# Optimization experiments

Hardware: AMD Instinct MI355X
Metric: run time of the kernel (lower is better)

Reference implementation:

```python
import jax, jax.numpy as jnp
import numpy as np

N_QUBITS = 14
N_LAYERS = 6
BATCH = 512
DIM = 2 ** N_QUBITS

# Z expectation sign table: qubit 0 is the most-significant bit of the state index
_idx = np.arange(DIM)
_bits = np.stack([(_idx >> (N_QUBITS - 1 - q)) & 1 for q in range(N_QUBITS)])  # [n, DIM]
SIGNS = jnp.asarray(1.0 - 2.0 * _bits, dtype=jnp.float32)  # +1 for bit 0, -1 for bit 1


def _rx(theta):
    # 2x2 RX(theta) = [[cos(t/2), -i sin(t/2)], [-i sin(t/2), cos(t/2)]]
    c = jnp.cos(theta / 2).astype(jnp.complex64)
    s = ((-1j) * jnp.sin(theta / 2)).astype(jnp.complex64)
    return jnp.stack([jnp.stack([c, s]), jnp.stack([s, c])])


def _apply_1q(state, mat, q):
    # state: [B, 2^n] complex; apply 2x2 mat on qubit q
    left = 2 ** q
    right = 2 ** (N_QUBITS - 1 - q)
    s = state.reshape(-1, left, 2, right)
    s = jnp.einsum('ij,bljr->blir', mat, s)
    return s.reshape(-1, DIM)


def _apply_cnot(state, c, t):
    # CNOT(control=c, target=t): flip target bit where control bit is 1
    hi, lo = (c, t) if c < t else (t, c)
    A = 2 ** hi
    M = 2 ** (lo - hi - 1)
    R = 2 ** (N_QUBITS - 1 - lo)
    s = state.reshape(-1, A, 2, M, 2, R)
    if c < t:
        flipped = jnp.flip(s[:, :, 1:2, :, :, :], axis=4)
        s = jnp.concatenate([s[:, :, 0:1, :, :, :], flipped], axis=2)
    else:
        flipped = jnp.flip(s[:, :, :, :, 1:2, :], axis=2)
        s = jnp.concatenate([s[:, :, :, :, 0:1, :], flipped], axis=4)
    return s.reshape(-1, DIM)


def _forward(x, params):
    B = x.shape[0]
    # angle embedding in X basis: product state of RX(x_q)|0> per qubit
    half = 0.5 * x
    amps = jnp.stack([jnp.cos(half).astype(jnp.complex64),
                      ((-1j) * jnp.sin(half)).astype(jnp.complex64)], axis=-1)  # [B, n, 2]
    state = amps[:, 0]
    for q in range(1, N_QUBITS):
        state = (state[:, :, None] * amps[:, q][:, None, :]).reshape(B, -1)
    # basic_entangling ansatz: per-qubit RX then ring of CNOTs, per layer
    for layer in range(N_LAYERS):
        w = params[layer, 0]  # [n_qubits]
        for q in range(N_QUBITS):
            state = _apply_1q(state, _rx(w[q]), q)
        for q in range(N_QUBITS):
            state = _apply_cnot(state, q, (q + 1) % N_QUBITS)
    # <Z_q> expectation per qubit
    probs = state.real ** 2 + state.imag ** 2  # [B, DIM]
    return probs @ SIGNS.T  # [B, n_qubits]


def setup_inputs():
    key = jax.random.key(0)
    k1, k2 = jax.random.split(key)
    x = jax.random.normal(k1, (BATCH, N_QUBITS), dtype=jnp.float32)
    params = 2.0 * jnp.pi * jax.random.uniform(k2, (N_LAYERS, 1, N_QUBITS), dtype=jnp.float32)
    return {"x": x, "params": params}


def reference(x, params):
    return _forward(x, params)
```

## Files before the change

kernel.cpp:

```cpp
#include <hip/hip_runtime.h>
#include <math.h>


#define NQ 14
#define DIM 16384
#define NLAYERS 6
#define NGATES (NLAYERS * NQ)
#define BATCH 512
#define TB 1024
#define NREP 16
#define NSLICE 16
#define SLICE_B (BATCH / NSLICE)
#define B_PER_WAVE (SLICE_B * 64 / TB)
static_assert(B_PER_WAVE == 2, "phase B hand-unrolled for 2 batches/wave");

constexpr int cpopc(unsigned v) { int c = 0; while (v) { c += (int)(v & 1u); v >>= 1; } return c; }

constexpr unsigned cpext(unsigned v, unsigned m) {
    unsigned r = 0; int b = 0;
    for (int pos = 0; pos < 16; ++pos)
        if ((m >> pos) & 1u) { r |= ((v >> pos) & 1u) << b; ++b; }
    return r;
}

struct Tabs {
    unsigned short m[NGATES];
    unsigned short r[NQ];
    int p[NQ];
    int off[NQ + 1];
    unsigned char qb[NQ][NQ];
    int ng[NQ];
    unsigned short gmask[NQ][NGATES];
    unsigned char  gidx[NQ][NGATES];
};

constexpr Tabs gen_tabs() {
    Tabs T{};
    unsigned short C[NQ] = {}, R[NQ] = {};
    for (int q = 0; q < NQ; ++q) { C[q] = (unsigned short)(1u << (NQ - 1 - q)); R[q] = C[q]; }
    for (int l = 0; l < NLAYERS; ++l) {
        for (int q = 0; q < NQ; ++q) T.m[l * NQ + q] = C[q];
        for (int g = 0; g < NQ; ++g) {
            int t = (g + 1) % NQ;
            C[g] ^= C[t];
            R[t] ^= R[g];
        }
    }
    for (int q = 0; q < NQ; ++q) T.r[q] = R[q];
    for (int q = 0; q < NQ; ++q) {
        int cnt = 0;
        for (int pos = 0; pos < NQ; ++pos)
            if ((R[q] >> pos) & 1u) { T.qb[q][cnt] = (unsigned char)(NQ - 1 - pos); ++cnt; }
        T.p[q] = cnt;
    }
    T.off[0] = 0;
    for (int q = 0; q < NQ; ++q) T.off[q + 1] = T.off[q] + (1 << T.p[q]);
    for (int q = 0; q < NQ; ++q) {
        int n = 0;
        for (int g = 0; g < NGATES; ++g) {
            if (cpopc((unsigned)(T.m[g] & R[q])) & 1) {
                T.gmask[q][n] = T.m[g];
                T.gidx[q][n]  = (unsigned char)g;
                ++n;
            }
        }
        T.ng[q] = n;
    }
    return T;
}
constexpr Tabs TAB = gen_tabs();

constexpr int calc_maxp() { int m = 0; for (int q = 0; q < NQ; ++q) if (TAB.p[q] > m) m = TAB.p[q]; return m; }
constexpr int calc_minp() { int m = 99; for (int q = 0; q < NQ; ++q) if (TAB.p[q] < m) m = TAB.p[q]; return m; }
constexpr int MAXP  = calc_maxp();
constexpr int MINP  = calc_minp();
constexpr int TOTAL = TAB.off[NQ];
static_assert(MAXP <= 8, "u = t & (2^p-1) needs p <= 10; replicas sized for p <= 8");
static_assert(MINP >= 1, "r mask must be nonzero");

template<int Q, int I>
__device__ __forceinline__ void gates(const float* __restrict__ params, int t,
                                      float (&P)[16])
{
    if constexpr (I < TAB.ng[Q]) {
        constexpr unsigned r  = TAB.r[Q];
        constexpr unsigned nr = (~r) & 0x3FFFu;
        constexpr int      p  = TAB.p[Q];
        constexpr unsigned mg = TAB.gmask[Q][I];
        constexpr unsigned Ag = cpext(mg, r);
        constexpr unsigned Bg = cpext(mg, nr);
        constexpr unsigned Mg = Ag | ((Bg & ((1u << (10 - p)) - 1u)) << p);
        constexpr unsigned Hg = (Bg >> (10 - p)) & 15u;
        const float th = params[(int)TAB.gidx[Q][I]];
        P[Hg] += (__popc((unsigned)t & Mg) & 1) ? -th : th;
        gates<Q, I + 1>(params, t, P);
    }
}

template<int Q>
__device__ __forceinline__ void build_q(const float* __restrict__ params,
                                        float* __restrict__ binC,
                                        float* __restrict__ binS, int t)
{
    constexpr int      p       = TAB.p[Q];
    constexpr unsigned lowmask = (1u << p) - 1u;

    float P[16];
    #pragma unroll
    for (int h = 0; h < 16; ++h) P[h] = 0.0f;
    gates<Q, 0>(params, t, P);

    #pragma unroll
    for (int s = 1; s < 8; s <<= 1) {
        #pragma unroll
        for (int h = 0; h < 16; ++h) {
            if (!(h & s)) {
                const int h1 = h | s;
                const float a = P[h], b = P[h1];
                P[h]  = a + b;
                P[h1] = a - b;
            }
        }
    }

    float fx = 0.0f, fy = 0.0f;
    #pragma unroll
    for (int h = 0; h < 8; ++h) {
        float sa, ca;
        __sincosf(P[h], &sa, &ca);
        const float cb = __cosf(P[h | 8]);
        fx = fmaf(cb, ca, fx);
        fy = fmaf(cb, sa, fy);
    }
    fx *= 2.0f; fy *= 2.0f;

    const unsigned u   = (unsigned)t & lowmask;
    const int      rep = t >> 6;
    float* bc = binC + (rep << MAXP);
    float* bs = binS + (rep << MAXP);

    if constexpr (p >= 6) {
        bc[u] = fx;
        bs[u] = fy;
    } else {
        constexpr unsigned dm = 63u & ~lowmask;
        #pragma unroll
        for (int bb = p; bb < 6; ++bb) {
            fx += __shfl_xor(fx, 1 << bb, 64);
            fy += __shfl_xor(fy, 1 << bb, 64);
        }
        if (((unsigned)t & dm) == 0u) {
            bc[u] = fx;
            bs[u] = fy;
        }
    }
}

template<int Q>
__device__ __forceinline__ void run_q(const float* __restrict__ params,
                                      float* __restrict__ binC,
                                      float* __restrict__ binS,
                                      float2* __restrict__ tab2,
                                      const float* __restrict__ sxAll,
                                      float* __restrict__ out,
                                      int slice, int t)
{
    build_q<Q>(params, binC, binS, t);
    __syncthreads();

    constexpr int p  = TAB.p[Q];
    constexpr int nb = 1 << p;
    if constexpr (p >= 6) {
        constexpr int STRIDE = 1 << (p - 6);
        constexpr int NW     = NREP / STRIDE;
        for (int i = t; i < nb; i += TB) {
            const int r0 = i >> 6;
            float sc = 0.0f, ss = 0.0f;
            #pragma unroll
            for (int c = 0; c < NW; ++c) {
                const int rp = r0 + c * STRIDE;
                sc += binC[(rp << MAXP) + i];
                ss += binS[(rp << MAXP) + i];
            }
            tab2[i] = make_float2(sc, ss);
        }
    } else {
        for (int i = t; i < nb; i += TB) {
            float sc = 0.0f, ss = 0.0f;
            #pragma unroll
            for (int rp = 0; rp < NREP; ++rp) {
                sc += binC[(rp << MAXP) + i];
                ss += binS[(rp << MAXP) + i];
            }
            tab2[i] = make_float2(sc, ss);
        }
    }
    __syncthreads();

    const int wave = t >> 6;
    const int lane = t & 63;
    const int bl0  = wave * B_PER_WAVE;
    const float* xr0 = sxAll + bl0 * NQ;
    const float* xr1 = xr0 + NQ;

    float acc0 = 0.0f, acc1 = 0.0f;
    if constexpr (p >= 6) {
        float xv0[p], xv1[p];
        #pragma unroll
        for (int i = 0; i < p; ++i) {
            xv0[i] = xr0[TAB.qb[Q][i]];
            xv1[i] = xr1[TAB.qb[Q][i]];
        }
        float A0 = 0.0f, A1 = 0.0f;
        #pragma unroll
        for (int i = 0; i < 6; ++i) {
            const bool bset = (lane >> i) & 1;
            A0 += bset ? xv0[i] : -xv0[i];
            A1 += bset ? xv1[i] : -xv1[i];
        }
        constexpr int HI = 1 << (p - 6);
        #pragma unroll
        for (int j = 0; j < HI; ++j) {
            float Aj0 = A0, Aj1 = A1;
            #pragma unroll
            for (int i = 6; i < p; ++i) {
                const bool bset = (j >> (i - 6)) & 1;
                Aj0 += bset ? xv0[i] : -xv0[i];
                Aj1 += bset ? xv1[i] : -xv1[i];
            }
            const float2 tv = tab2[lane + (j << 6)];
            float s0, c0, s1, c1;
            __sincosf(Aj0, &s0, &c0);
            __sincosf(Aj1, &s1, &c1);
            acc0 = fmaf(c0, tv.x, fmaf(s0, tv.y, acc0));
            acc1 = fmaf(c1, tv.x, fmaf(s1, tv.y, acc1));
        }
    } else {
        if (lane < nb) {
            float A0 = 0.0f, A1 = 0.0f;
            #pragma unroll
            for (int i = 0; i < p; ++i) {
                const bool bset = (lane >> i) & 1;
                const float x0 = xr0[TAB.qb[Q][i]];
                const float x1 = xr1[TAB.qb[Q][i]];
                A0 += bset ? x0 : -x0;
                A1 += bset ? x1 : -x1;
            }
            const float2 tv = tab2[lane];
            float s0, c0, s1, c1;
            __sincosf(A0, &s0, &c0);
            __sincosf(A1, &s1, &c1);
            acc0 = fmaf(c0, tv.x, fmaf(s0, tv.y, acc0));
            acc1 = fmaf(c1, tv.x, fmaf(s1, tv.y, acc1));
        }
    }

    #pragma unroll
    for (int o = 32; o > 0; o >>= 1) {
        acc0 += __shfl_down(acc0, o, 64);
        acc1 += __shfl_down(acc1, o, 64);
    }
    if (lane == 0) {
        out[(slice * SLICE_B + bl0)     * NQ + Q] = acc0 * (1.0f / (float)DIM);
        out[(slice * SLICE_B + bl0 + 1) * NQ + Q] = acc1 * (1.0f / (float)DIM);
    }
}

__global__ __launch_bounds__(TB, 4)
void fused_kernel(const float* __restrict__ x, const float* __restrict__ params,
                  float* __restrict__ out)
{
    __shared__ float  binC[NREP << MAXP];
    __shared__ float  binS[NREP << MAXP];
    __shared__ float2 tab2[1 << MAXP];
    __shared__ float  sxAll[SLICE_B * NQ];

    const int q     = blockIdx.x % NQ;
    const int slice = blockIdx.x / NQ;
    const int t     = threadIdx.x;

    for (int i = t; i < SLICE_B * NQ; i += TB) sxAll[i] = x[slice * (SLICE_B * NQ) + i];

    switch (q) {
        case 0:  run_q<0 >(params, binC, binS, tab2, sxAll, out, slice, t); break;
        case 1:  run_q<1 >(params, binC, binS, tab2, sxAll, out, slice, t); break;
        case 2:  run_q<2 >(params, binC, binS, tab2, sxAll, out, slice, t); break;
        case 3:  run_q<3 >(params, binC, binS, tab2, sxAll, out, slice, t); break;
        case 4:  run_q<4 >(params, binC, binS, tab2, sxAll, out, slice, t); break;
        case 5:  run_q<5 >(params, binC, binS, tab2, sxAll, out, slice, t); break;
        case 6:  run_q<6 >(params, binC, binS, tab2, sxAll, out, slice, t); break;
        case 7:  run_q<7 >(params, binC, binS, tab2, sxAll, out, slice, t); break;
        case 8:  run_q<8 >(params, binC, binS, tab2, sxAll, out, slice, t); break;
        case 9:  run_q<9 >(params, binC, binS, tab2, sxAll, out, slice, t); break;
        case 10: run_q<10>(params, binC, binS, tab2, sxAll, out, slice, t); break;
        case 11: run_q<11>(params, binC, binS, tab2, sxAll, out, slice, t); break;
        case 12: run_q<12>(params, binC, binS, tab2, sxAll, out, slice, t); break;
        case 13: run_q<13>(params, binC, binS, tab2, sxAll, out, slice, t); break;
    }
}

extern "C" void kernel_launch(void* const* d_in, const int* in_sizes, int n_in,
                              void* d_out, int out_size, void* d_ws, size_t ws_size,
                              hipStream_t stream) {
    const float* x      = (const float*)d_in[0];
    const float* params = (const float*)d_in[1];
    float* out          = (float*)d_out;
    (void)d_ws; (void)ws_size;

    fused_kernel<<<NQ * NSLICE, TB, 0, stream>>>(x, params, out);
}
```

Before: 57.29 us.

## Precompute gate sign bitmasks, pack bins as float2, permute inputs, DPP reductions

After: 56.47 us. About the same (-1.4%).

```diff
diff --git a/kernel.cpp b/kernel.cpp
--- a/kernel.cpp
+++ b/kernel.cpp
@@ -72,14 +72,86 @@
 
 constexpr int calc_maxp() { int m = 0; for (int q = 0; q < NQ; ++q) if (TAB.p[q] > m) m = TAB.p[q]; return m; }
 constexpr int calc_minp() { int m = 99; for (int q = 0; q < NQ; ++q) if (TAB.p[q] < m) m = TAB.p[q]; return m; }
+constexpr int calc_maxng() { int m = 0; for (int q = 0; q < NQ; ++q) if (TAB.ng[q] > m) m = TAB.ng[q]; return m; }
 constexpr int MAXP  = calc_maxp();
 constexpr int MINP  = calc_minp();
 constexpr int TOTAL = TAB.off[NQ];
 static_assert(MAXP <= 8, "u = t & (2^p-1) needs p <= 10; replicas sized for p <= 8");
 static_assert(MINP >= 1, "r mask must be nonzero");
+static_assert(calc_maxng() <= 64, "sign vector packed in one uint64");
+
+struct RMaps { unsigned m[NQ][NGATES]; };
+constexpr RMaps gen_rmap() {
+    RMaps M{};
+    for (int q = 0; q < NQ; ++q) {
+        const unsigned r  = TAB.r[q];
+        const unsigned nr = (~r) & 0x3FFFu;
+        const int      p  = TAB.p[q];
+        for (int n = 0; n < TAB.ng[q]; ++n) {
+            const unsigned mg = TAB.gmask[q][n];
+            const unsigned Ag = cpext(mg, r);
+            const unsigned Bg = cpext(mg, nr);
+            M.m[q][n] = Ag | ((Bg & ((1u << (10 - p)) - 1u)) << p);
+        }
+    }
+    return M;
+}
+constexpr RMaps RMAP = gen_rmap();
+
+struct Par64 { unsigned char v[64]; };
+constexpr Par64 gen_par64() {
+    Par64 P{};
+    for (int i = 0; i < 64; ++i) {
+        unsigned x = (unsigned)i;
+        x ^= x >> 4; x ^= x >> 2; x ^= x >> 1;
+        P.v[i] = (unsigned char)(x & 1u);
+    }
+    return P;
+}
+constexpr Par64 PAR = gen_par64();
+
+struct SignLuts {
+    unsigned long long lane[NQ][64];
+    unsigned long long wave[NQ][16];
+};
+constexpr SignLuts gen_luts() {
+    SignLuts L{};
+    for (int q = 0; q < NQ; ++q) {
+        for (int ln = 0; ln < 64; ++ln) {
+            unsigned long long v = 0;
+            for (int n = 0; n < TAB.ng[q]; ++n)
+                if (PAR.v[(unsigned)ln & (RMAP.m[q][n] & 63u)]) v |= 1ull << n;
+            L.lane[q][ln] = v;
+        }
+        for (int wd = 0; wd < 16; ++wd) {
+            unsigned long long v = 0;
+            for (int n = 0; n < TAB.ng[q]; ++n)
+                if (PAR.v[(unsigned)wd & (RMAP.m[q][n] >> 6)]) v |= 1ull << n;
+            L.wave[q][wd] = v;
+        }
+    }
+    return L;
+}
+constexpr SignLuts SLUT = gen_luts();
+
+template<int CTRL>
+__device__ __forceinline__ float dpp_add(float v) {
+    const int s = __builtin_amdgcn_update_dpp(0, __float_as_int(v), CTRL, 0xf, 0xf, true);
+    return v + __int_as_float(s);
+}
+__device__ __forceinline__ float wave64_sum(float v) {
+    v = dpp_add<0x111>(v);
+    v = dpp_add<0x112>(v);
+    v = dpp_add<0x114>(v);
+    v = dpp_add<0x118>(v);
+    v = dpp_add<0x142>(v);
+    v = dpp_add<0x143>(v);
+    return v;
+}
 
 template<int Q, int I>
-__device__ __forceinline__ void gates(const float* __restrict__ params, int t,
+__device__ __forceinline__ void gates(const float* __restrict__ params,
+                                      unsigned svLo, unsigned svHi,
                                       float (&P)[16])
 {
     if constexpr (I < TAB.ng[Q]) {
@@ -87,28 +159,33 @@
         constexpr unsigned nr = (~r) & 0x3FFFu;
         constexpr int      p  = TAB.p[Q];
         constexpr unsigned mg = TAB.gmask[Q][I];
-        constexpr unsigned Ag = cpext(mg, r);
         constexpr unsigned Bg = cpext(mg, nr);
-        constexpr unsigned Mg = Ag | ((Bg & ((1u << (10 - p)) - 1u)) << p);
         constexpr unsigned Hg = (Bg >> (10 - p)) & 15u;
         const float th = params[(int)TAB.gidx[Q][I]];
-        P[Hg] += (__popc((unsigned)t & Mg) & 1) ? -th : th;
-        gates<Q, I + 1>(params, t, P);
+        const unsigned svh = (I < 32) ? svLo : svHi;
+        const unsigned sgn = (svh << (31 - (I & 31))) & 0x80000000u;
+        P[Hg] += __uint_as_float(__float_as_uint(th) ^ sgn);
+        gates<Q, I + 1>(params, svLo, svHi, P);
     }
 }
 
 template<int Q>
 __device__ __forceinline__ void build_q(const float* __restrict__ params,
-                                        float* __restrict__ binC,
-                                        float* __restrict__ binS, int t)
+                                        float2* __restrict__ bins2, int t)
 {
     constexpr int      p       = TAB.p[Q];
     constexpr unsigned lowmask = (1u << p) - 1u;
 
+    const int lane = t & 63;
+    const int wid  = t >> 6;
+    const unsigned long long sv = SLUT.lane[Q][lane] ^ SLUT.wave[Q][wid];
+    const unsigned svLo = (unsigned)sv;
+    const unsigned svHi = (unsigned)(sv >> 32);
+
     float P[16];
     #pragma unroll
     for (int h = 0; h < 16; ++h) P[h] = 0.0f;
-    gates<Q, 0>(params, t, P);
+    gates<Q, 0>(params, svLo, svHi, P);
 
     #pragma unroll
     for (int s = 1; s < 8; s <<= 1) {
@@ -132,16 +209,12 @@
         fx = fmaf(cb, ca, fx);
         fy = fmaf(cb, sa, fy);
     }
-    fx *= 2.0f; fy *= 2.0f;
-
-    const unsigned u   = (unsigned)t & lowmask;
-    const int      rep = t >> 6;
-    float* bc = binC + (rep << MAXP);
-    float* bs = binS + (rep << MAXP);
+
+    const unsigned u = (unsigned)t & lowmask;
+    float2* bp = bins2 + (wid << MAXP);
 
     if constexpr (p >= 6) {
-        bc[u] = fx;
-        bs[u] = fy;
+        bp[u] = make_float2(fx, fy);
     } else {
         constexpr unsigned dm = 63u & ~lowmask;
         #pragma unroll
@@ -150,22 +223,20 @@
             fy += __shfl_xor(fy, 1 << bb, 64);
         }
         if (((unsigned)t & dm) == 0u) {
-            bc[u] = fx;
-            bs[u] = fy;
+            bp[u] = make_float2(fx, fy);
         }
     }
 }
 
 template<int Q>
 __device__ __forceinline__ void run_q(const float* __restrict__ params,
-                                      float* __restrict__ binC,
-                                      float* __restrict__ binS,
+                                      float2* __restrict__ bins2,
                                       float2* __restrict__ tab2,
-                                      const float* __restrict__ sxAll,
+                                      const float4* __restrict__ sxPerm4,
                                       float* __restrict__ out,
                                       int slice, int t)
 {
-    build_q<Q>(params, binC, binS, t);
+    build_q<Q>(params, bins2, t);
     __syncthreads();
 
     constexpr int p  = TAB.p[Q];
@@ -178,9 +249,8 @@
             float sc = 0.0f, ss = 0.0f;
             #pragma unroll
             for (int c = 0; c < NW; ++c) {
-                const int rp = r0 + c * STRIDE;
-                sc += binC[(rp << MAXP) + i];
-                ss += binS[(rp << MAXP) + i];
+                const float2 v = bins2[((r0 + c * STRIDE) << MAXP) + i];
+                sc += v.x; ss += v.y;
             }
             tab2[i] = make_float2(sc, ss);
         }
@@ -189,8 +259,8 @@
             float sc = 0.0f, ss = 0.0f;
             #pragma unroll
             for (int rp = 0; rp < NREP; ++rp) {
-                sc += binC[(rp << MAXP) + i];
-                ss += binS[(rp << MAXP) + i];
+                const float2 v = bins2[(rp << MAXP) + i];
+                sc += v.x; ss += v.y;
             }
             tab2[i] = make_float2(sc, ss);
         }
@@ -200,17 +270,14 @@
     const int wave = t >> 6;
     const int lane = t & 63;
     const int bl0  = wave * B_PER_WAVE;
-    const float* xr0 = sxAll + bl0 * NQ;
-    const float* xr1 = xr0 + NQ;
+
+    const float4 a0 = sxPerm4[bl0 * 2],       b0 = sxPerm4[bl0 * 2 + 1];
+    const float4 a1 = sxPerm4[(bl0 + 1) * 2], b1 = sxPerm4[(bl0 + 1) * 2 + 1];
+    const float xv0[8] = {a0.x, a0.y, a0.z, a0.w, b0.x, b0.y, b0.z, b0.w};
+    const float xv1[8] = {a1.x, a1.y, a1.z, a1.w, b1.x, b1.y, b1.z, b1.w};
 
     float acc0 = 0.0f, acc1 = 0.0f;
     if constexpr (p >= 6) {
-        float xv0[p], xv1[p];
-        #pragma unroll
-        for (int i = 0; i < p; ++i) {
-            xv0[i] = xr0[TAB.qb[Q][i]];
-            xv1[i] = xr1[TAB.qb[Q][i]];
-        }
         float A0 = 0.0f, A1 = 0.0f;
         #pragma unroll
         for (int i = 0; i < 6; ++i) {
@@ -241,10 +308,8 @@
             #pragma unroll
             for (int i = 0; i < p; ++i) {
                 const bool bset = (lane >> i) & 1;
-                const float x0 = xr0[TAB.qb[Q][i]];
-                const float x1 = xr1[TAB.qb[Q][i]];
-                A0 += bset ? x0 : -x0;
-                A1 += bset ? x1 : -x1;
+                A0 += bset ? xv0[i] : -xv0[i];
+                A1 += bset ? xv1[i] : -xv1[i];
             }
             const float2 tv = tab2[lane];
             float s0, c0, s1, c1;
@@ -255,14 +320,12 @@
         }
     }
 
-    #pragma unroll
-    for (int o = 32; o > 0; o >>= 1) {
-        acc0 += __shfl_down(acc0, o, 64);
-        acc1 += __shfl_down(acc1, o, 64);
-    }
-    if (lane == 0) {
-        out[(slice * SLICE_B + bl0)     * NQ + Q] = acc0 * (1.0f / (float)DIM);
-        out[(slice * SLICE_B + bl0 + 1) * NQ + Q] = acc1 * (1.0f / (float)DIM);
+    acc0 = wave64_sum(acc0);
+    acc1 = wave64_sum(acc1);
+    if (lane == 63) {
+        constexpr float SCALE = 2.0f / (float)DIM;
+        out[(slice * SLICE_B + bl0)     * NQ + Q] = acc0 * SCALE;
+        out[(slice * SLICE_B + bl0 + 1) * NQ + Q] = acc1 * SCALE;
     }
 }
 
@@ -270,32 +333,38 @@
 void fused_kernel(const float* __restrict__ x, const float* __restrict__ params,
                   float* __restrict__ out)
 {
-    __shared__ float  binC[NREP << MAXP];
-    __shared__ float  binS[NREP << MAXP];
+    __shared__ float2 bins2[NREP << MAXP];
     __shared__ float2 tab2[1 << MAXP];
-    __shared__ float  sxAll[SLICE_B * NQ];
+    __shared__ float4 sxPerm4[SLICE_B * 2];
 
     const int q     = blockIdx.x % NQ;
     const int slice = blockIdx.x / NQ;
     const int t     = threadIdx.x;
 
-    for (int i = t; i < SLICE_B * NQ; i += TB) sxAll[i] = x[slice * (SLICE_B * NQ) + i];
+    float* sp = (float*)sxPerm4;
+    for (int i = t; i < SLICE_B * 8; i += TB) {
+        const int b = i >> 3, j = i & 7;
+        float v = 0.0f;
+        if (j < TAB.p[q])
+            v = x[(slice * SLICE_B + b) * NQ + (int)TAB.qb[q][j]];
+        sp[i] = v;
+    }
 
     switch (q) {
-        case 0:  run_q<0 >(params, binC, binS, tab2, sxAll, out, slice, t); break;
-        case 1:  run_q<1 >(params, binC, binS, tab2, sxAll, out, slice, t); break;
-        case 2:  run_q<2 >(params, binC, binS, tab2, sxAll, out, slice, t); break;
-        case 3:  run_q<3 >(params, binC, binS, tab2, sxAll, out, slice, t); break;
-        case 4:  run_q<4 >(params, binC, binS, tab2, sxAll, out, slice, t); break;
-        case 5:  run_q<5 >(params, binC, binS, tab2, sxAll, out, slice, t); break;
-        case 6:  run_q<6 >(params, binC, binS, tab2, sxAll, out, slice, t); break;
-        case 7:  run_q<7 >(params, binC, binS, tab2, sxAll, out, slice, t); break;
-        case 8:  run_q<8 >(params, binC, binS, tab2, sxAll, out, slice, t); break;
-        case 9:  run_q<9 >(params, binC, binS, tab2, sxAll, out, slice, t); break;
-        case 10: run_q<10>(params, binC, binS, tab2, sxAll, out, slice, t); break;
-        case 11: run_q<11>(params, binC, binS, tab2, sxAll, out, slice, t); break;
-        case 12: run_q<12>(params, binC, binS, tab2, sxAll, out, slice, t); break;
-        case 13: run_q<13>(params, binC, binS, tab2, sxAll, out, slice, t); break;
+        case 0:  run_q<0 >(params, bins2, tab2, sxPerm4, out, slice, t); break;
+        case 1:  run_q<1 >(params, bins2, tab2, sxPerm4, out, slice, t); break;
+        case 2:  run_q<2 >(params, bins2, tab2, sxPerm4, out, slice, t); break;
+        case 3:  run_q<3 >(params, bins2, tab2, sxPerm4, out, slice, t); break;
+        case 4:  run_q<4 >(params, bins2, tab2, sxPerm4, out, slice, t); break;
+        case 5:  run_q<5 >(params, bins2, tab2, sxPerm4, out, slice, t); break;
+        case 6:  run_q<6 >(params, bins2, tab2, sxPerm4, out, slice, t); break;
+        case 7:  run_q<7 >(params, bins2, tab2, sxPerm4, out, slice, t); break;
+        case 8:  run_q<8 >(params, bins2, tab2, sxPerm4, out, slice, t); break;
+        case 9:  run_q<9 >(params, bins2, tab2, sxPerm4, out, slice, t); break;
+        case 10: run_q<10>(params, bins2, tab2, sxPerm4, out, slice, t); break;
+        case 11: run_q<11>(params, bins2, tab2, sxPerm4, out, slice, t); break;
+        case 12: run_q<12>(params, bins2, tab2, sxPerm4, out, slice, t); break;
+        case 13: run_q<13>(params, bins2, tab2, sxPerm4, out, slice, t); break;
     }
 }
 
```
